# Optimization experiments

Measured on AMD Instinct MI355X. Metric: run time of the kernel, lower is better.

The kernel has to match this reference:

```python
import jax, jax.numpy as jnp
import numpy as np
import math

EMBED = 768
N_HEAD = 12
HEAD = EMBED // N_HEAD
RADIUS = 128
POS_SIZE = 2 * RADIUS
B, S = 8, 1024


def setup_inputs() -> dict:
    key = jax.random.key(0)
    ks = jax.random.split(key, 6)
    x = jax.random.normal(ks[0], (B, S, EMBED), dtype=jnp.float32)
    # torch Linear weights have shape [out, in]; y = x @ W.T
    Wq = jax.random.normal(ks[1], (EMBED, EMBED), dtype=jnp.float32) * 0.02
    Wk = jax.random.normal(ks[2], (EMBED, EMBED), dtype=jnp.float32) * 0.02
    Wv = jax.random.normal(ks[3], (EMBED, EMBED), dtype=jnp.float32) * 0.02
    Wp = jax.random.normal(ks[4], (EMBED, EMBED), dtype=jnp.float32) * 0.02
    pos_emb_k = jax.random.normal(ks[5], (POS_SIZE, HEAD), dtype=jnp.float32) * 0.02
    return {"x": x, "Wq": Wq, "Wk": Wk, "Wv": Wv, "Wp": Wp, "pos_emb_k": pos_emb_k}


def reference(x, Wq, Wk, Wv, Wp, pos_emb_k):
    b, s, e = x.shape
    # projections -> [B, H, S, D]
    def split_heads(t):
        return t.reshape(b, s, N_HEAD, HEAD).transpose(0, 2, 1, 3)
    q = split_heads(x @ Wq.T)
    k = split_heads(x @ Wk.T)
    v = split_heads(x @ Wv.T)
    # relative-position logits: [B, H, S, 2R]
    att_rel_pos = jnp.einsum('bhsd,pd->bhsp', q, pos_emb_k)
    # index map: clamp(j - i, -R, R-1) mod 2R -> [S, S]
    rel = jnp.arange(s)[None, :] - jnp.arange(s)[:, None]
    att_idxs = jnp.clip(rel, -RADIUS, RADIUS - 1) % POS_SIZE
    idxs = jnp.broadcast_to(att_idxs[None, None], (b, N_HEAD, s, s))
    att_pos = jnp.take_along_axis(att_rel_pos, idxs, axis=3)  # [B, H, S, S]
    att_val = jnp.einsum('bhqd,bhkd->bhqk', q, k)
    att = jax.nn.softmax((att_val + att_pos) * (1.0 / math.sqrt(HEAD)), axis=-1)
    y = jnp.einsum('bhqk,bhkd->bhqd', att, v)
    y = y.transpose(0, 2, 1, 3).reshape(b, s, e)
    return y @ Wp.T
```

## Files before the change

### kernel.cpp

```cpp
#include <hip/hip_runtime.h>

#define NB 8
#define NS 1024
#define NE 768
#define NH 12
#define ND 64

typedef __attribute__((ext_vector_type(8))) short bf16x8;
typedef __attribute__((ext_vector_type(4))) float f32x4;
typedef __attribute__((ext_vector_type(16))) float f32x16;
typedef const __attribute__((address_space(1))) void gv_t;
typedef __attribute__((address_space(3))) void sv_t;

static __device__ __forceinline__ ushort f2bf(float f) {
  union { float f; unsigned u; } c; c.f = f;
  unsigned u = c.u + 0x7fffu + ((c.u >> 16) & 1u);
  return (ushort)(u >> 16);
}
static __device__ __forceinline__ float bf2f(ushort h) {
  union { unsigned u; float f; } c; c.u = ((unsigned)h) << 16;
  return c.f;
}
static __device__ __forceinline__ uint pk_bf16(float lo, float hi) {
  uint r;
  asm("v_cvt_pk_bf16_f32 %0, %1, %2" : "=v"(r) : "v"(lo), "v"(hi));
  return r;
}
#define PL32SWAP(a, b) asm("v_permlane32_swap_b32 %0, %1" : "+v"(a), "+v"(b))
#define GLDS16(src, dst) __builtin_amdgcn_global_load_lds((gv_t*)(src), (sv_t*)(dst), 16, 0, 0)

__global__ void cvt_x(const float* __restrict__ src, ushort* __restrict__ dst) {
  int i = (blockIdx.x * 256 + threadIdx.x) * 4;
  float4 f = *(const float4*)(src + i);
  ushort4 o;
  o.x = f2bf(f.x); o.y = f2bf(f.y); o.z = f2bf(f.z); o.w = f2bf(f.w);
  *(ushort4*)(dst + i) = o;
}

__global__ void cvt_weights(const float* __restrict__ w0, const float* __restrict__ w1,
                            const float* __restrict__ w2, const float* __restrict__ w3,
                            const float* __restrict__ w4,
                            ushort* __restrict__ o0, ushort* __restrict__ o1,
                            ushort* __restrict__ o2, ushort* __restrict__ o3,
                            ushort* __restrict__ o4) {
  int blk = blockIdx.x;
  const float* src; ushort* dst; int idx;
  if (blk < 2304) {
    int ws = blk / 576, b = blk % 576;
    src = (ws == 0) ? w0 : (ws == 1) ? w1 : (ws == 2) ? w2 : w3;
    dst = (ws == 0) ? o0 : (ws == 1) ? o1 : (ws == 2) ? o2 : o3;
    idx = b;
  } else {
    src = w4; dst = o4; idx = blk - 2304;
  }
  int i = (idx * 256 + threadIdx.x) * 4;
  float4 f = *(const float4*)(src + i);
  ushort4 o;
  o.x = f2bf(f.x); o.y = f2bf(f.y); o.z = f2bf(f.z); o.w = f2bf(f.w);
  *(ushort4*)(dst + i) = o;
}

__device__ __forceinline__ void gemm_core(const ushort* __restrict__ A,
                                          const ushort* __restrict__ Bw,
                                          ushort* As, ushort* Bs,
                                          int bm0, int bn0, f32x4 (&acc)[4][4]) {
  const int tid = threadIdx.x;
  const int w = tid >> 6, lane = tid & 63;
  const int l15 = lane & 15, l4 = lane >> 4;
  const int wm = w >> 1, wn = w & 1;
  const int row = tid >> 2, seg = tid & 3;

  #pragma unroll 1
  for (int kt = 0; kt < 24; ++kt) {
    __syncthreads();
    #pragma unroll
    for (int p = 0; p < 2; ++p) {
      const ushort* ga = A + (size_t)(bm0 + p * 64 + row) * 768 + kt * 32 + seg * 8;
      GLDS16(ga, As + (p * 256 + w * 64) * 8);
      const ushort* gb = Bw + (size_t)(bn0 + p * 64 + row) * 768 + kt * 32 + seg * 8;
      GLDS16(gb, Bs + (p * 256 + w * 64) * 8);
    }
    __syncthreads();

    bf16x8 af[4], bf[4];
    #pragma unroll
    for (int mi = 0; mi < 4; ++mi)
      af[mi] = *(const bf16x8*)(As + (wm * 64 + mi * 16 + l15) * 32 + l4 * 8);
    #pragma unroll
    for (int ni = 0; ni < 4; ++ni)
      bf[ni] = *(const bf16x8*)(Bs + (wn * 64 + ni * 16 + l15) * 32 + l4 * 8);
    #pragma unroll
    for (int mi = 0; mi < 4; ++mi)
      #pragma unroll
      for (int ni = 0; ni < 4; ++ni)
        acc[mi][ni] = __builtin_amdgcn_mfma_f32_16x16x32_bf16(af[mi], bf[ni], acc[mi][ni], 0, 0, 0);
  }
}

__global__ __launch_bounds__(256)
void gemm_qkv(const ushort* __restrict__ A,
              const ushort* __restrict__ B0, const ushort* __restrict__ B1, const ushort* __restrict__ B2,
              ushort* __restrict__ C0, ushort* __restrict__ C1, ushort* __restrict__ C2) {
  __shared__ __align__(16) char gsm[34816];
  ushort* As = (ushort*)gsm;
  ushort* Bs = As + 4096;
  ushort* VtS = (ushort*)gsm;

  const int wsel = blockIdx.y / 6;
  const int bn0 = (blockIdx.y % 6) * 128;
  const int bm0 = blockIdx.x * 128;
  const ushort* Bw = (wsel == 0) ? B0 : (wsel == 1) ? B1 : B2;
  ushort* Co = (wsel == 0) ? C0 : (wsel == 1) ? C1 : C2;

  f32x4 acc[4][4];
  #pragma unroll
  for (int i = 0; i < 4; ++i)
    #pragma unroll
    for (int j = 0; j < 4; ++j)
      acc[i][j] = (f32x4){0.f, 0.f, 0.f, 0.f};

  gemm_core(A, Bw, As, Bs, bm0, bn0, acc);

  const int tid = threadIdx.x;
  const int lane = tid & 63;
  const int w = tid >> 6;
  const int l15 = lane & 15, l4 = lane >> 4;
  const int wm = w >> 1, wn = w & 1;

  if (wsel == 2) {
    __syncthreads();
    #pragma unroll
    for (int mi = 0; mi < 4; ++mi) {
      #pragma unroll
      for (int ni = 0; ni < 4; ++ni) {
        const int nl = wn * 64 + ni * 16 + l15;
        const int ml = wm * 64 + mi * 16 + l4 * 4;
        ushort4 pk;
        pk.x = f2bf(acc[mi][ni][0]); pk.y = f2bf(acc[mi][ni][1]);
        pk.z = f2bf(acc[mi][ni][2]); pk.w = f2bf(acc[mi][ni][3]);
        *(ushort4*)&VtS[nl * 136 + ml] = pk;
      }
    }
    __syncthreads();
    #pragma unroll
    for (int p = 0; p < 8; ++p) {
      const int n = p * 16 + (tid >> 4);
      const int m = (tid & 15) * 8;
      bf16x8 vv = *(const bf16x8*)&VtS[n * 136 + m];
      const int ng = bn0 + n, h = ng >> 6, d = ng & 63;
      const int mg = bm0 + m, b = mg >> 10, sl = mg & 1023;
      size_t off = (size_t)(b * NH + h) * 65536 + (size_t)(sl >> 5) * 2048
                 + (size_t)((d >> 5) * 2 + ((sl >> 4) & 1)) * 512
                 + ((sl >> 3) & 1) * 256 + (d & 31) * 8;
      *(bf16x8*)&Co[off] = vv;
    }
  } else if (wsel == 1) {
    #pragma unroll
    for (int mi = 0; mi < 4; ++mi) {
      #pragma unroll
      for (int ni = 0; ni < 4; ++ni) {
        #pragma unroll
        for (int e = 0; e < 4; ++e) {
          int m = bm0 + wm * 64 + mi * 16 + l4 * 4 + e;
          int n = bn0 + wn * 64 + ni * 16 + l15;
          int b = m >> 10, s = m & 1023, h = n >> 6, d = n & 63;
          size_t off = (size_t)(b * NH + h) * 65536 + (size_t)(s >> 5) * 2048
                     + (size_t)(d >> 4) * 512 + ((d >> 3) & 1) * 256
                     + (s & 31) * 8 + (d & 7);
          Co[off] = f2bf(acc[mi][ni][e]);
        }
      }
    }
  } else {
    const float scl = 0.18033688f;
    #pragma unroll
    for (int mi = 0; mi < 4; ++mi) {
      #pragma unroll
      for (int ni = 0; ni < 4; ++ni) {
        #pragma unroll
        for (int e = 0; e < 4; ++e) {
          int m = bm0 + wm * 64 + mi * 16 + l4 * 4 + e;
          int n = bn0 + wn * 64 + ni * 16 + l15;
          int b = m >> 10, s = m & 1023, h = n >> 6, d = n & 63;
          Co[(size_t)(b * NH + h) * 65536 + (s << 6) + d] = f2bf(acc[mi][ni][e] * scl);
        }
      }
    }
  }
}

__global__ __launch_bounds__(256)
void gemm_proj(const ushort* __restrict__ A, const ushort* __restrict__ Bw,
               float* __restrict__ Cout) {
  __shared__ ushort As[128 * 32];
  __shared__ ushort Bs[128 * 32];
  const int bm0 = blockIdx.x * 128;
  const int bn0 = blockIdx.y * 128;

  f32x4 acc[4][4];
  #pragma unroll
  for (int i = 0; i < 4; ++i)
    #pragma unroll
    for (int j = 0; j < 4; ++j)
      acc[i][j] = (f32x4){0.f, 0.f, 0.f, 0.f};

  gemm_core(A, Bw, As, Bs, bm0, bn0, acc);

  const int lane = threadIdx.x & 63;
  const int w = threadIdx.x >> 6;
  const int l15 = lane & 15, l4 = lane >> 4;
  const int wm = w >> 1, wn = w & 1;
  #pragma unroll
  for (int mi = 0; mi < 4; ++mi) {
    #pragma unroll
    for (int ni = 0; ni < 4; ++ni) {
      #pragma unroll
      for (int e = 0; e < 4; ++e) {
        int m = bm0 + wm * 64 + mi * 16 + l4 * 4 + e;
        int n = bn0 + wn * 64 + ni * 16 + l15;
        Cout[(size_t)m * NE + n] = acc[mi][ni][e];
      }
    }
  }
}

#define FINISH_CHUNK(S, VF00, VF01, VF10, VF11)                               \
  {                                                                           \
    float m01 = fmaxf(S[0], S[1]),  m23 = fmaxf(S[2], S[3]);                  \
    float m45 = fmaxf(S[4], S[5]),  m67 = fmaxf(S[6], S[7]);                  \
    float m89 = fmaxf(S[8], S[9]),  mab = fmaxf(S[10], S[11]);                \
    float mcd = fmaxf(S[12], S[13]), mef = fmaxf(S[14], S[15]);               \
    float cmax = fmaxf(fmaxf(fmaxf(m01, m23), fmaxf(m45, m67)),               \
                       fmaxf(fmaxf(m89, mab), fmaxf(mcd, mef)));              \
    cmax = fmaxf(cmax, __shfl_xor(cmax, 32));                                 \
    const float m_new = fmaxf(m_run, cmax);                                   \
    if (__any(m_new - m_run > 8.f)) {                                         \
      const float sc = __builtin_amdgcn_exp2f(m_run - m_new);                 \
      l_run *= sc;                                                            \
      m_run = m_new;                                                          \
      _Pragma("unroll")                                                       \
      for (int i = 0; i < 16; ++i) { o0[i] *= sc; o1[i] *= sc; }              \
    }                                                                         \
    float ls = 0.f;                                                           \
    _Pragma("unroll")                                                         \
    for (int i = 0; i < 16; ++i) {                                            \
      S[i] = __builtin_amdgcn_exp2f(S[i] - m_run);                            \
      ls += S[i];                                                             \
    }                                                                         \
    l_run += ls;                                                              \
    uint a0 = pk_bf16(S[0],  S[1]);                                           \
    uint a1 = pk_bf16(S[2],  S[3]);                                           \
    uint a2 = pk_bf16(S[4],  S[5]);                                           \
    uint a3 = pk_bf16(S[6],  S[7]);                                           \
    uint a4 = pk_bf16(S[8],  S[9]);                                           \
    uint a5 = pk_bf16(S[10], S[11]);                                          \
    uint a6 = pk_bf16(S[12], S[13]);                                          \
    uint a7 = pk_bf16(S[14], S[15]);                                          \
    PL32SWAP(a0, a2);                                                         \
    PL32SWAP(a1, a3);                                                         \
    PL32SWAP(a4, a6);                                                         \
    PL32SWAP(a5, a7);                                                         \
    union FU { bf16x8 v; uint u[4]; } f0, f1;                                 \
    f0.u[0] = a0; f0.u[1] = a1; f0.u[2] = a2; f0.u[3] = a3;                   \
    f1.u[0] = a4; f1.u[1] = a5; f1.u[2] = a6; f1.u[3] = a7;                   \
    __builtin_amdgcn_s_setprio(1);                                            \
    o0 = __builtin_amdgcn_mfma_f32_32x32x16_bf16(VF00, f0.v, o0, 0, 0, 0);    \
    o0 = __builtin_amdgcn_mfma_f32_32x32x16_bf16(VF01, f1.v, o0, 0, 0, 0);    \
    o1 = __builtin_amdgcn_mfma_f32_32x32x16_bf16(VF10, f0.v, o1, 0, 0, 0);    \
    o1 = __builtin_amdgcn_mfma_f32_32x32x16_bf16(VF11, f1.v, o1, 0, 0, 0);    \
    __builtin_amdgcn_s_setprio(0);                                            \
  }

static __device__ __forceinline__ f32x16 bias_init(int dlt, const ushort* RlRow,
                                                   float c_lo, float c_hi,
                                                   int half4, int il) {
  f32x16 s;
  if (dlt <= -160 || dlt >= 160) {
    const float cv = (dlt < 0) ? c_lo : c_hi;
    #pragma unroll
    for (int i = 0; i < 16; ++i) s[i] = cv;
  } else {
    #pragma unroll
    for (int i = 0; i < 16; ++i) {
      const int rr = (i & 3) + 8 * (i >> 2) + half4;
      int rel = dlt + rr - il;
      rel = rel < -128 ? -128 : (rel > 127 ? 127 : rel);
      s[i] = bf2f(RlRow[rel & 255]);
    }
  }
  return s;
}

#define LOADK(P, C)                                                           \
  k##P##0 = *(const bf16x8*)(kc + (C) * 2048);                                \
  k##P##1 = *(const bf16x8*)(kc + (C) * 2048 + 512);                          \
  k##P##2 = *(const bf16x8*)(kc + (C) * 2048 + 1024);                         \
  k##P##3 = *(const bf16x8*)(kc + (C) * 2048 + 1536);
#define LOADV(P, C)                                                           \
  v##P##0 = *(const bf16x8*)(vc + (C) * 2048);                                \
  v##P##1 = *(const bf16x8*)(vc + (C) * 2048 + 512);                          \
  v##P##2 = *(const bf16x8*)(vc + (C) * 2048 + 1024);                         \
  v##P##3 = *(const bf16x8*)(vc + (C) * 2048 + 1536);

#define CHUNK(C, P)                                                           \
  {                                                                           \
    f32x16 s = bias_init(w * 256 + (C) * 32 - q0, RlRow, c_lo, c_hi, half4, il); \
    __builtin_amdgcn_s_setprio(1);                                            \
    s = __builtin_amdgcn_mfma_f32_32x32x16_bf16(k##P##0, qf[0], s, 0, 0, 0);  \
    s = __builtin_amdgcn_mfma_f32_32x32x16_bf16(k##P##1, qf[1], s, 0, 0, 0);  \
    s = __builtin_amdgcn_mfma_f32_32x32x16_bf16(k##P##2, qf[2], s, 0, 0, 0);  \
    s = __builtin_amdgcn_mfma_f32_32x32x16_bf16(k##P##3, qf[3], s, 0, 0, 0);  \
    __builtin_amdgcn_s_setprio(0);                                            \
    if ((C) + 2 < 8) { LOADK(P, (C) + 2) }                                    \
    FINISH_CHUNK(s, v##P##0, v##P##1, v##P##2, v##P##3);                      \
    if ((C) + 2 < 8) { LOADV(P, (C) + 2) }                                    \
  }

__global__ __launch_bounds__(256, 3)
void attn_kernel(const ushort* __restrict__ q, const ushort* __restrict__ k4,
                 const ushort* __restrict__ v4, const ushort* __restrict__ pe,
                 ushort* __restrict__ y) {
  __shared__ __align__(16) char smem[17920];
  ushort* Rl = (ushort*)smem;
  float* OL  = (float*)smem;
  float* ML  = (float*)(smem + 16896);

  const int tid = threadIdx.x;
  const int w = tid >> 6, lane = tid & 63;
  const int il = lane & 31;
  const int hb = lane >> 5;
  const int hi8 = hb * 8;
  const int half4 = hb * 4;

  const int bid = blockIdx.x;
  const int swz_b = (bid & 7) * 384 + (bid >> 3);
  const int bh = swz_b >> 5;
  const int q0 = (swz_b & 31) * 32;

  const ushort* qp = q + (size_t)bh * 65536;
  const ushort* kc = k4 + (size_t)bh * 65536 + w * 16384 + lane * 8;
  const ushort* vc = v4 + (size_t)bh * 65536 + w * 16384 + lane * 8;

  bf16x8 qf[4];
  #pragma unroll
  for (int ks = 0; ks < 4; ++ks)
    qf[ks] = *(const bf16x8*)(qp + (q0 + il) * 64 + ks * 16 + hi8);

  bf16x8 ka0, ka1, ka2, ka3, va0, va1, va2, va3;
  bf16x8 kb0, kb1, kb2, kb3, vb0, vb1, vb2, vb3;
  LOADK(a, 0) LOADV(a, 0)
  LOADK(b, 1) LOADV(b, 1)

  #pragma unroll
  for (int pb = 0; pb < 2; ++pb) {
    const int pc0 = (w * 2 + pb) * 32;
    f32x16 r;
    #pragma unroll
    for (int i = 0; i < 16; ++i) r[i] = 0.f;
    #pragma unroll
    for (int ks = 0; ks < 4; ++ks) {
      bf16x8 pf = *(const bf16x8*)(pe + (pc0 + il) * 64 + ks * 16 + hi8);
      r = __builtin_amdgcn_mfma_f32_32x32x16_bf16(qf[ks], pf, r, 0, 0, 0);
    }
    #pragma unroll
    for (int i = 0; i < 16; ++i) {
      const int rr = (i & 3) + 8 * (i >> 2) + half4;
      Rl[rr * 258 + pc0 + il] = f2bf(r[i]);
    }
  }
  __syncthreads();

  const ushort* RlRow = Rl + il * 258;
  const float c_lo = bf2f(RlRow[128]);
  const float c_hi = bf2f(RlRow[127]);

  float m_run = -1e30f, l_run = 0.f;
  f32x16 o0, o1;
  #pragma unroll
  for (int i = 0; i < 16; ++i) { o0[i] = 0.f; o1[i] = 0.f; }

  CHUNK(0, a)
  CHUNK(1, b)
  CHUNK(2, a)
  CHUNK(3, b)
  CHUNK(4, a)
  CHUNK(5, b)
  CHUNK(6, a)
  CHUNK(7, b)

  l_run += __shfl_xor(l_run, 32);

  __syncthreads();
  #pragma unroll
  for (int i = 0; i < 16; ++i) {
    const int rr = (i & 3) + 8 * (i >> 2) + half4;
    OL[(w * 32 + rr) * 33 + il] = o0[i];
  }
  if (hb == 0) {
    ML[(w * 2) * 32 + il] = m_run;
    ML[(w * 2 + 1) * 32 + il] = l_run;
  }
  __syncthreads();

  const int mq = tid >> 3;
  const int dg = (tid & 7) * 4;
  float mw[4], lw[4];
  #pragma unroll
  for (int wv = 0; wv < 4; ++wv) {
    mw[wv] = ML[(wv * 2) * 32 + mq];
    lw[wv] = ML[(wv * 2 + 1) * 32 + mq];
  }
  const float ms = fmaxf(fmaxf(mw[0], mw[1]), fmaxf(mw[2], mw[3]));
  float cw[4], lst = 0.f;
  #pragma unroll
  for (int wv = 0; wv < 4; ++wv) {
    cw[wv] = __builtin_amdgcn_exp2f(mw[wv] - ms);
    lst += cw[wv] * lw[wv];
  }
  const float inv = 1.f / lst;

  float r0[4] = {0.f, 0.f, 0.f, 0.f};
  #pragma unroll
  for (int wv = 0; wv < 4; ++wv)
    #pragma unroll
    for (int e = 0; e < 4; ++e)
      r0[e] += cw[wv] * OL[(wv * 32 + dg + e) * 33 + mq];

  __syncthreads();
  #pragma unroll
  for (int i = 0; i < 16; ++i) {
    const int rr = (i & 3) + 8 * (i >> 2) + half4;
    OL[(w * 32 + rr) * 33 + il] = o1[i];
  }
  __syncthreads();

  float r1[4] = {0.f, 0.f, 0.f, 0.f};
  #pragma unroll
  for (int wv = 0; wv < 4; ++wv)
    #pragma unroll
    for (int e = 0; e < 4; ++e)
      r1[e] += cw[wv] * OL[(wv * 32 + dg + e) * 33 + mq];

  const int b = bh / NH, h = bh % NH;
  ushort* yrow = y + (size_t)(b * NS + q0 + mq) * NE + h * 64;
  ushort4 s0, s1;
  s0.x = f2bf(r0[0] * inv); s0.y = f2bf(r0[1] * inv);
  s0.z = f2bf(r0[2] * inv); s0.w = f2bf(r0[3] * inv);
  s1.x = f2bf(r1[0] * inv); s1.y = f2bf(r1[1] * inv);
  s1.z = f2bf(r1[2] * inv); s1.w = f2bf(r1[3] * inv);
  *(ushort4*)(yrow + dg) = s0;
  *(ushort4*)(yrow + 32 + dg) = s1;
}

extern "C" void kernel_launch(void* const* d_in, const int* in_sizes, int n_in,
                              void* d_out, int out_size, void* d_ws, size_t ws_size,
                              hipStream_t stream) {
  const float* x  = (const float*)d_in[0];
  const float* Wq = (const float*)d_in[1];
  const float* Wk = (const float*)d_in[2];
  const float* Wv = (const float*)d_in[3];
  const float* Wp = (const float*)d_in[4];
  const float* pe = (const float*)d_in[5];

  ushort* ws  = (ushort*)d_ws;
  ushort* xb  = ws;
  ushort* wqb = xb  + 6291456;
  ushort* wkb = wqb + 589824;
  ushort* wvb = wkb + 589824;
  ushort* wpb = wvb + 589824;
  ushort* peb = wpb + 589824;
  ushort* qb  = peb + 16384;
  ushort* k4b = qb  + 6291456;
  ushort* v4b = k4b + 6291456;
  ushort* yb  = v4b + 6291456;

  cvt_x<<<dim3(6144), dim3(256), 0, stream>>>(x, xb);
  cvt_weights<<<dim3(2320), dim3(256), 0, stream>>>(Wq, Wk, Wv, Wp, pe,
                                                    wqb, wkb, wvb, wpb, peb);
  gemm_qkv<<<dim3(64, 18), dim3(256), 0, stream>>>(xb, wqb, wkb, wvb, qb, k4b, v4b);
  attn_kernel<<<dim3(3072), dim3(256), 0, stream>>>(qb, k4b, v4b, peb, yb);
  gemm_proj<<<dim3(64, 6), dim3(256), 0, stream>>>(yb, wpb, (float*)d_out);
}
```

Measured before the change: 154.4 us.

## Double-buffer GEMM LDS tiles and merge conversion kernels into one launch

The shared GEMM core now uses two LDS buffers and issues the global-to-LDS loads for the next K tile before computing on the current one. This cuts the syncs per iteration from two to one and overlaps load latency with MFMA work. The x and weight conversion kernels are also merged into a single launch to save launch overhead. It doubles LDS use in gemm_proj, which fits inside gemm_qkv's existing buffer, and that may reduce occupancy.

```diff
diff --git a/kernel.cpp b/kernel.cpp
--- a/kernel.cpp
+++ b/kernel.cpp
@@ -29,29 +29,26 @@
 #define PL32SWAP(a, b) asm("v_permlane32_swap_b32 %0, %1" : "+v"(a), "+v"(b))
 #define GLDS16(src, dst) __builtin_amdgcn_global_load_lds((gv_t*)(src), (sv_t*)(dst), 16, 0, 0)
 
-__global__ void cvt_x(const float* __restrict__ src, ushort* __restrict__ dst) {
-  int i = (blockIdx.x * 256 + threadIdx.x) * 4;
-  float4 f = *(const float4*)(src + i);
-  ushort4 o;
-  o.x = f2bf(f.x); o.y = f2bf(f.y); o.z = f2bf(f.z); o.w = f2bf(f.w);
-  *(ushort4*)(dst + i) = o;
-}
-
-__global__ void cvt_weights(const float* __restrict__ w0, const float* __restrict__ w1,
-                            const float* __restrict__ w2, const float* __restrict__ w3,
-                            const float* __restrict__ w4,
-                            ushort* __restrict__ o0, ushort* __restrict__ o1,
-                            ushort* __restrict__ o2, ushort* __restrict__ o3,
-                            ushort* __restrict__ o4) {
+__global__ void cvt_all(const float* __restrict__ x,
+                        const float* __restrict__ w0, const float* __restrict__ w1,
+                        const float* __restrict__ w2, const float* __restrict__ w3,
+                        const float* __restrict__ w4,
+                        ushort* __restrict__ xd,
+                        ushort* __restrict__ o0, ushort* __restrict__ o1,
+                        ushort* __restrict__ o2, ushort* __restrict__ o3,
+                        ushort* __restrict__ o4) {
   int blk = blockIdx.x;
   const float* src; ushort* dst; int idx;
-  if (blk < 2304) {
-    int ws = blk / 576, b = blk % 576;
+  if (blk < 6144) {
+    src = x; dst = xd; idx = blk;
+  } else if (blk < 8448) {
+    int b = blk - 6144;
+    int ws = b / 576;
     src = (ws == 0) ? w0 : (ws == 1) ? w1 : (ws == 2) ? w2 : w3;
     dst = (ws == 0) ? o0 : (ws == 1) ? o1 : (ws == 2) ? o2 : o3;
-    idx = b;
+    idx = b % 576;
   } else {
-    src = w4; dst = o4; idx = blk - 2304;
+    src = w4; dst = o4; idx = blk - 8448;
   }
   int i = (idx * 256 + threadIdx.x) * 4;
   float4 f = *(const float4*)(src + i);
@@ -62,7 +59,7 @@
 
 __device__ __forceinline__ void gemm_core(const ushort* __restrict__ A,
                                           const ushort* __restrict__ Bw,
-                                          ushort* As, ushort* Bs,
+                                          ushort* S0,
                                           int bm0, int bn0, f32x4 (&acc)[4][4]) {
   const int tid = threadIdx.x;
   const int w = tid >> 6, lane = tid & 63;
@@ -70,18 +67,25 @@
   const int wm = w >> 1, wn = w & 1;
   const int row = tid >> 2, seg = tid & 3;
 
-  #pragma unroll 1
+#define STAGE_KT(KT, B)                                                        \
+  { ushort* As_ = S0 + (B) * 8192; ushort* Bs_ = As_ + 4096;                   \
+    _Pragma("unroll")                                                          \
+    for (int p = 0; p < 2; ++p) {                                              \
+      const ushort* ga = A + (size_t)(bm0 + p * 64 + row) * 768 + (KT) * 32 + seg * 8; \
+      GLDS16(ga, As_ + (p * 256 + w * 64) * 8);                                \
+      const ushort* gb = Bw + (size_t)(bn0 + p * 64 + row) * 768 + (KT) * 32 + seg * 8; \
+      GLDS16(gb, Bs_ + (p * 256 + w * 64) * 8);                                \
+    } }
+
+  STAGE_KT(0, 0)
+  __syncthreads();
+
+  #pragma unroll 2
   for (int kt = 0; kt < 24; ++kt) {
-    __syncthreads();
-    #pragma unroll
-    for (int p = 0; p < 2; ++p) {
-      const ushort* ga = A + (size_t)(bm0 + p * 64 + row) * 768 + kt * 32 + seg * 8;
-      GLDS16(ga, As + (p * 256 + w * 64) * 8);
-      const ushort* gb = Bw + (size_t)(bn0 + p * 64 + row) * 768 + kt * 32 + seg * 8;
-      GLDS16(gb, Bs + (p * 256 + w * 64) * 8);
-    }
-    __syncthreads();
-
+    if (kt < 23) { STAGE_KT(kt + 1, (kt + 1) & 1) }
+
+    ushort* As = S0 + (kt & 1) * 8192;
+    ushort* Bs = As + 4096;
     bf16x8 af[4], bf[4];
     #pragma unroll
     for (int mi = 0; mi < 4; ++mi)
@@ -94,7 +98,10 @@
       #pragma unroll
       for (int ni = 0; ni < 4; ++ni)
         acc[mi][ni] = __builtin_amdgcn_mfma_f32_16x16x32_bf16(af[mi], bf[ni], acc[mi][ni], 0, 0, 0);
-  }
+
+    __syncthreads();
+  }
+#undef STAGE_KT
 }
 
 __global__ __launch_bounds__(256)
@@ -102,8 +109,7 @@
               const ushort* __restrict__ B0, const ushort* __restrict__ B1, const ushort* __restrict__ B2,
               ushort* __restrict__ C0, ushort* __restrict__ C1, ushort* __restrict__ C2) {
   __shared__ __align__(16) char gsm[34816];
-  ushort* As = (ushort*)gsm;
-  ushort* Bs = As + 4096;
+  ushort* S0 = (ushort*)gsm;
   ushort* VtS = (ushort*)gsm;
 
   const int wsel = blockIdx.y / 6;
@@ -119,7 +125,7 @@
     for (int j = 0; j < 4; ++j)
       acc[i][j] = (f32x4){0.f, 0.f, 0.f, 0.f};
 
-  gemm_core(A, Bw, As, Bs, bm0, bn0, acc);
+  gemm_core(A, Bw, S0, bm0, bn0, acc);
 
   const int tid = threadIdx.x;
   const int lane = tid & 63;
@@ -192,8 +198,7 @@
 __global__ __launch_bounds__(256)
 void gemm_proj(const ushort* __restrict__ A, const ushort* __restrict__ Bw,
                float* __restrict__ Cout) {
-  __shared__ ushort As[128 * 32];
-  __shared__ ushort Bs[128 * 32];
+  __shared__ __align__(16) ushort S0[16384];
   const int bm0 = blockIdx.x * 128;
   const int bn0 = blockIdx.y * 128;
 
@@ -204,7 +209,7 @@
     for (int j = 0; j < 4; ++j)
       acc[i][j] = (f32x4){0.f, 0.f, 0.f, 0.f};
 
-  gemm_core(A, Bw, As, Bs, bm0, bn0, acc);
+  gemm_core(A, Bw, S0, bm0, bn0, acc);
 
   const int lane = threadIdx.x & 63;
   const int w = threadIdx.x >> 6;
@@ -474,9 +479,8 @@
   ushort* v4b = k4b + 6291456;
   ushort* yb  = v4b + 6291456;
 
-  cvt_x<<<dim3(6144), dim3(256), 0, stream>>>(x, xb);
-  cvt_weights<<<dim3(2320), dim3(256), 0, stream>>>(Wq, Wk, Wv, Wp, pe,
-                                                    wqb, wkb, wvb, wpb, peb);
+  cvt_all<<<dim3(8464), dim3(256), 0, stream>>>(x, Wq, Wk, Wv, Wp, pe,
+                                                xb, wqb, wkb, wvb, wpb, peb);
   gemm_qkv<<<dim3(64, 18), dim3(256), 0, stream>>>(xb, wqb, wkb, wvb, qb, k4b, v4b);
   attn_kernel<<<dim3(3072), dim3(256), 0, stream>>>(qb, k4b, v4b, peb, yb);
   gemm_proj<<<dim3(64, 6), dim3(256), 0, stream>>>(yb, wpb, (float*)d_out);
```

New measurement: 138.7 us. -10.2%, faster.
